# Performance work log

Measured on AMD Instinct MI355X. Metric: run time of the kernel, lower is better.

The kernel has to match this reference:

```python
import jax, jax.numpy as jnp
import numpy as np

N_HEAD = 16


def _rope_cache(T, head_dim):
    half = head_dim // 2
    inv_freq = 1.0 / (10000.0 ** (jnp.arange(half, dtype=jnp.float32) / half))
    t = jnp.arange(T, dtype=jnp.float32)
    freqs = jnp.einsum('i,j->ij', t, inv_freq)            # (T, half)
    cos = jnp.repeat(jnp.cos(freqs), 2, axis=-1)          # (T, head_dim)
    sin = jnp.repeat(jnp.sin(freqs), 2, axis=-1)
    return cos, sin


def _apply_rope(x, cos, sin):
    # x: (B, H, T, D); cos/sin: (T, D)
    x1 = x[..., ::2]
    x2 = x[..., 1::2]
    x_rot = jnp.stack([-x2, x1], axis=-1).reshape(x.shape)
    return x * cos[None, None] + x_rot * sin[None, None]


def setup_inputs() -> dict:
    key = jax.random.key(0)
    k1, k2, k3 = jax.random.split(key, 3)
    B, T, C = 2, 2048, 1024
    x = jax.random.normal(k1, (B, T, C), dtype=jnp.float32)
    Wqkv = jax.random.normal(k2, (C, 3 * C), dtype=jnp.float32) * 0.02
    Wo = jax.random.normal(k3, (C, C), dtype=jnp.float32) * 0.02
    bo = jnp.zeros((C,), dtype=jnp.float32)
    return {"x": x, "Wqkv": Wqkv, "Wo": Wo, "bo": bo}


def reference(x, Wqkv, Wo, bo):
    B, T, C = x.shape
    H = N_HEAD
    D = C // H
    scale = D ** -0.5

    qkv = x @ Wqkv                                        # (B, T, 3C)
    qkv = qkv.reshape(B, T, 3, H, D).transpose(2, 0, 3, 1, 4)  # (3, B, H, T, D)
    q, k, v = qkv[0], qkv[1], qkv[2]

    cos, sin = _rope_cache(T, D)
    q = _apply_rope(q, cos, sin)
    k = _apply_rope(k, cos, sin)

    att = jnp.einsum('bhqd,bhkd->bhqk', q, k) * scale     # (B, H, T, T)
    causal = jnp.tril(jnp.ones((T, T), dtype=bool))
    att = jnp.where(causal[None, None], att, -jnp.inf)
    att = jax.nn.softmax(att, axis=-1)                    # dropout is identity in eval

    out = jnp.einsum('bhqk,bhkd->bhqd', att, v)           # (B, H, T, D)
    out = out.transpose(0, 2, 1, 3).reshape(B, T, C)
    return out @ Wo + bo
```

## Files before the change

### kernel.cpp

```cpp
#include <hip/hip_runtime.h>

typedef __attribute__((ext_vector_type(8))) short bf16x8;
typedef __attribute__((ext_vector_type(4))) float f32x4;
typedef __attribute__((ext_vector_type(4))) unsigned uint32x4;

#define MFMA32(a, b, c) __builtin_amdgcn_mfma_f32_16x16x32_bf16((a), (b), (c), 0, 0, 0)

__device__ __forceinline__ unsigned short f2bf(float f) {
  unsigned u = __builtin_bit_cast(unsigned, f);
  u += 0x7fffu + ((u >> 16) & 1u);
  return (unsigned short)(u >> 16);
}
__device__ __forceinline__ unsigned pack2(float a, float b) {
  return (unsigned)f2bf(a) | ((unsigned)f2bf(b) << 16);
}
__device__ __forceinline__ unsigned pack2t(float lo, float hi) {
  return __builtin_amdgcn_perm(__builtin_bit_cast(unsigned, hi),
                               __builtin_bit_cast(unsigned, lo), 0x07060302u);
}
__device__ __forceinline__ void gl_lds16(const unsigned short* g, unsigned short* l) {
  __builtin_amdgcn_global_load_lds(
      (const __attribute__((address_space(1))) unsigned int*)(g),
      (__attribute__((address_space(3))) unsigned int*)(l), 16, 0, 0);
}

#define QSCALE 0.18033688011112042f

__global__ __launch_bounds__(256) void prep_kernel(
    const float* __restrict__ x, const float* __restrict__ Wqkv,
    const float* __restrict__ Wo, unsigned short* __restrict__ xb,
    unsigned short* __restrict__ wqt, unsigned short* __restrict__ wot) {
  __shared__ unsigned short Tl[64][72];
  const int bid = blockIdx.x, tid = threadIdx.x;
  if (bid < 2048) {
    int i = (bid * 256 + tid) * 8;
    float4 a = *(const float4*)(x + i);
    float4 b = *(const float4*)(x + i + 4);
    uint4 w;
    w.x = pack2(a.x, a.y); w.y = pack2(a.z, a.w);
    w.z = pack2(b.x, b.y); w.w = pack2(b.z, b.w);
    *(uint4*)(xb + i) = w;
  } else {
    const float* src;
    unsigned short* dst;
    int N, kt, nt;
    if (bid < 2816) {
      int r = bid - 2048;
      src = Wqkv; dst = wqt; N = 3072;
      nt = (r % 48) * 64; kt = (r / 48) * 64;
    } else {
      int r = bid - 2816;
      src = Wo; dst = wot; N = 1024;
      nt = (r & 15) * 64; kt = (r >> 4) * 64;
    }
    const int rr = tid >> 2, cs = (tid & 3) * 16;
    const float* sp = src + (kt + rr) * N + nt + cs;
    uint4 w0, w1;
    {
      float4 a = *(const float4*)(sp), b = *(const float4*)(sp + 4);
      float4 c = *(const float4*)(sp + 8), d = *(const float4*)(sp + 12);
      w0.x = pack2(a.x, a.y); w0.y = pack2(a.z, a.w);
      w0.z = pack2(b.x, b.y); w0.w = pack2(b.z, b.w);
      w1.x = pack2(c.x, c.y); w1.y = pack2(c.z, c.w);
      w1.z = pack2(d.x, d.y); w1.w = pack2(d.z, d.w);
    }
    *(uint4*)(&Tl[rr][cs]) = w0;
    *(uint4*)(&Tl[rr][cs + 8]) = w1;
    __syncthreads();
    unsigned short tmp[16];
#pragma unroll
    for (int i = 0; i < 16; i++) tmp[i] = Tl[cs + i][rr];
    unsigned short* dp = dst + (nt + rr) * 1024 + kt + cs;
    *(uint4*)(dp) = *(const uint4*)(&tmp[0]);
    *(uint4*)(dp + 8) = *(const uint4*)(&tmp[8]);
  }
}

__global__ __launch_bounds__(256, 6) void qkv_rope_kernel(
    const unsigned short* __restrict__ xb, const unsigned short* __restrict__ wt,
    unsigned short* __restrict__ qws, unsigned short* __restrict__ kws,
    unsigned short* __restrict__ vws) {
  __shared__ unsigned short Al[2 * 64 * 32];
  __shared__ unsigned short Bl[2 * 128 * 32];

  const int tid = threadIdx.x;
  const int lane = tid & 63, wid = tid >> 6;
  const int quad = lane >> 4, col = lane & 15;
  const int wm = (wid >> 1) * 32, wn = (wid & 1) * 64;
  const int n0 = blockIdx.x * 128, m0 = blockIdx.y * 64;

  f32x4 acc[2][4] = {};
  const int srA = wid * 16 + (lane >> 2);
  const int srB = wid * 32 + (lane >> 2);
  const int gseg = ((lane & 3) ^ ((lane >> 3) & 3)) * 8;
  const int fsg = (quad ^ ((col >> 1) & 3)) * 8;

  for (int k0 = 0; k0 < 1024; k0 += 64) {
#pragma unroll
    for (int c = 0; c < 2; c++) {
      const int kc = k0 + c * 32;
      gl_lds16(xb + (m0 + srA) * 1024 + kc + gseg, Al + c * 2048 + (wid * 16) * 32);
      gl_lds16(wt + (n0 + srB) * 1024 + kc + gseg, Bl + c * 4096 + (wid * 32) * 32);
      gl_lds16(wt + (n0 + srB + 16) * 1024 + kc + gseg,
               Bl + c * 4096 + (wid * 32 + 16) * 32);
    }
    __syncthreads();

#pragma unroll
    for (int c = 0; c < 2; c++) {
      bf16x8 af[2], bfr[4];
#pragma unroll
      for (int i = 0; i < 2; i++)
        af[i] = *(const bf16x8*)(&Al[c * 2048 + (wm + i * 16 + col) * 32 + fsg]);
#pragma unroll
      for (int j = 0; j < 4; j++)
        bfr[j] = *(const bf16x8*)(&Bl[c * 4096 + (wn + j * 16 + col) * 32 + fsg]);
#pragma unroll
      for (int i = 0; i < 2; i++)
#pragma unroll
        for (int j = 0; j < 4; j++)
          acc[i][j] = MFMA32(af[i], bfr[j], acc[i][j]);
    }
    __syncthreads();
  }

#pragma unroll
  for (int i = 0; i < 2; i++) {
#pragma unroll
    for (int j = 0; j < 4; j++) {
      const int nbase = n0 + wn + j * 16;
      const int region = nbase >> 10;
#pragma unroll
      for (int r = 0; r < 4; r++) {
        int m = m0 + wm + i * 16 + quad * 4 + r;
        int n = nbase + col;
        float val = acc[i][j][r];
        int nn = n & 1023, h = nn >> 6, d = nn & 63, b = m >> 11, t = m & 2047;
        if (region < 2) {
          float other = __shfl_xor(val, 1);
          float invf = __expf(-(float)(d >> 1) * 0.28782313662425572f);
          float ang = (float)t * invf;
          float sn, cs;
          __sincosf(ang, &sn, &cs);
          float rot = (d & 1) ? other : -other;
          val = fmaf(val, cs, rot * sn);
        }
        int bh = (b << 4) + h;
        if (region == 0) {
          qws[(bh * 2048 + t) * 64 + d] = f2bf(val * QSCALE);
        } else if (region == 1) {
          kws[(bh * 2048 + t) * 64 + d] = f2bf(val);
        } else {
          int tl = t & 31, g = t >> 5;
          int qd = (tl & 15) >> 2;
          int jj = (tl & 3) + ((tl & 16) ? 4 : 0);
          int tp = g * 32 + qd * 8 + jj;
          vws[(bh * 64 + d) * 2048 + tp] = f2bf(val);
        }
      }
    }
  }
}

__global__ __launch_bounds__(256, 4) void attn_kernel(
    const unsigned short* __restrict__ qws, const unsigned short* __restrict__ kws,
    const unsigned short* __restrict__ vws, unsigned short* __restrict__ aws) {
  __shared__ unsigned short Kl[2][64 * 64];
  __shared__ unsigned short Vl[2][64 * 64];

  const int tid = threadIdx.x;
  const int lane = tid & 63, wid = tid >> 6;
  const int quad = lane >> 4, col = lane & 15;
  const int bh = blockIdx.x;
  const unsigned short* qb = qws + bh * (2048 * 64);
  const unsigned short* kb = kws + bh * (2048 * 64);
  const unsigned short* vb = vws + bh * (64 * 2048);
  const int b = bh >> 4, h = bh & 15;

  const int sro = wid * 16 + (lane >> 3);
  const int sgs = ((lane & 7) ^ ((lane >> 3) & 7)) * 8;
  const int sA = (quad ^ (col & 7)) * 8;

  const int q0blk = (31 - (int)blockIdx.y) * 64;
  const int qt = q0blk + wid * 16;
  const int qi = qt + col;
  const int qi_max = qt + 15;
  const int kend = q0blk + 64;

  bf16x8 qf0 = *(const bf16x8*)(qb + (qt + col) * 64 + quad * 8);
  bf16x8 qf1 = *(const bf16x8*)(qb + (qt + col) * 64 + 32 + quad * 8);

  f32x4 o[4] = {};
  float lsum = 0.f;

  for (int k0 = 0; k0 < kend; k0 += 128) {
    const int nsub = (kend - k0 > 64) ? 2 : 1;
    for (int u = 0; u < nsub; u++) {
      const int kb0 = k0 + u * 64;
      gl_lds16(kb + (kb0 + sro) * 64 + sgs, Kl[u] + (wid * 16) * 64);
      gl_lds16(kb + (kb0 + sro + 8) * 64 + sgs, Kl[u] + (wid * 16 + 8) * 64);
      gl_lds16(vb + sro * 2048 + kb0 + sgs, Vl[u] + (wid * 16) * 64);
      gl_lds16(vb + (sro + 8) * 2048 + kb0 + sgs, Vl[u] + (wid * 16 + 8) * 64);
    }
    __syncthreads();

    for (int u = 0; u < nsub; u++) {
      const int kb0 = k0 + u * 64;
      if (kb0 > qi_max) break;
      const int smax = min(4, ((qi_max - kb0) >> 4) + 1);
      const bool diag = (kb0 + 64 > qt);
      float p[16];
#pragma unroll
      for (int s = 0; s < 4; s++) {
        if (s < smax) {
          bf16x8 kfa = *(const bf16x8*)(&Kl[u][(s * 16 + col) * 64 + sA]);
          bf16x8 kfb = *(const bf16x8*)(&Kl[u][(s * 16 + col) * 64 + (sA ^ 32)]);
          f32x4 z = {0.f, 0.f, 0.f, 0.f};
          z = MFMA32(kfa, qf0, z);
          z = MFMA32(kfb, qf1, z);
          if (diag) {
#pragma unroll
            for (int r = 0; r < 4; r++)
              if (kb0 + s * 16 + quad * 4 + r > qi) z[r] = -1e30f;
          }
#pragma unroll
          for (int r = 0; r < 4; r++) {
            float e = exp2f(z[r]);
            p[s * 4 + r] = e;
            lsum += e;
          }
        } else {
#pragma unroll
          for (int r = 0; r < 4; r++) p[s * 4 + r] = 0.f;
        }
      }
      uint32x4 u0;
      u0[0] = pack2t(p[0], p[1]);   u0[1] = pack2t(p[2], p[3]);
      u0[2] = pack2t(p[4], p[5]);   u0[3] = pack2t(p[6], p[7]);
      bf16x8 pf0 = __builtin_bit_cast(bf16x8, u0);
#pragma unroll
      for (int dt = 0; dt < 4; dt++) {
        bf16x8 vfa = *(const bf16x8*)(&Vl[u][(dt * 16 + col) * 64 + sA]);
        o[dt] = MFMA32(vfa, pf0, o[dt]);
      }
      if (smax > 2) {
        uint32x4 u1;
        u1[0] = pack2t(p[8], p[9]);   u1[1] = pack2t(p[10], p[11]);
        u1[2] = pack2t(p[12], p[13]); u1[3] = pack2t(p[14], p[15]);
        bf16x8 pf1 = __builtin_bit_cast(bf16x8, u1);
#pragma unroll
        for (int dt = 0; dt < 4; dt++) {
          bf16x8 vfb = *(const bf16x8*)(&Vl[u][(dt * 16 + col) * 64 + (sA ^ 32)]);
          o[dt] = MFMA32(vfb, pf1, o[dt]);
        }
      }
    }
    __syncthreads();
  }

  lsum += __shfl_xor(lsum, 16);
  lsum += __shfl_xor(lsum, 32);
  float inv = 1.0f / lsum;
#pragma unroll
  for (int dt = 0; dt < 4; dt++)
#pragma unroll
    for (int r = 0; r < 4; r++) {
      int d = dt * 16 + quad * 4 + r;
      aws[(b * 2048 + qt + col) * 1024 + h * 64 + d] = f2bf(o[dt][r] * inv);
    }
}

__global__ __launch_bounds__(256) void out_proj_kernel(
    const unsigned short* __restrict__ attn, const unsigned short* __restrict__ wot,
    const float* __restrict__ bo, float* __restrict__ out) {
  __shared__ unsigned short Al[2 * 64 * 32];
  __shared__ unsigned short Bl[2 * 128 * 32];

  const int tid = threadIdx.x;
  const int lane = tid & 63, wid = tid >> 6;
  const int quad = lane >> 4, col = lane & 15;
  const int wm = (wid >> 1) * 32, wn = (wid & 1) * 64;
  const int n0 = blockIdx.x * 128, m0 = blockIdx.y * 64;

  f32x4 acc[2][4] = {};
  const int sr = lane >> 2;
  const int gseg = ((lane & 3) ^ ((lane >> 3) & 3)) * 8;
  const int fsg = (quad ^ ((col >> 1) & 3)) * 8;

  for (int k0 = 0; k0 < 1024; k0 += 64) {
#pragma unroll
    for (int c = 0; c < 2; c++) {
      const int kc = k0 + c * 32;
      gl_lds16(attn + (m0 + wid * 16 + sr) * 1024 + kc + gseg,
               Al + c * 2048 + (wid * 16) * 32);
      gl_lds16(wot + (n0 + wid * 32 + sr) * 1024 + kc + gseg,
               Bl + c * 4096 + (wid * 32) * 32);
      gl_lds16(wot + (n0 + wid * 32 + 16 + sr) * 1024 + kc + gseg,
               Bl + c * 4096 + (wid * 32 + 16) * 32);
    }
    __syncthreads();

#pragma unroll
    for (int c = 0; c < 2; c++) {
      bf16x8 af[2], bfr[4];
#pragma unroll
      for (int i = 0; i < 2; i++)
        af[i] = *(const bf16x8*)(&Al[c * 2048 + (wm + i * 16 + col) * 32 + fsg]);
#pragma unroll
      for (int j = 0; j < 4; j++)
        bfr[j] = *(const bf16x8*)(&Bl[c * 4096 + (wn + j * 16 + col) * 32 + fsg]);
#pragma unroll
      for (int i = 0; i < 2; i++)
#pragma unroll
        for (int j = 0; j < 4; j++)
          acc[i][j] = MFMA32(af[i], bfr[j], acc[i][j]);
    }
    __syncthreads();
  }

#pragma unroll
  for (int i = 0; i < 2; i++)
#pragma unroll
    for (int j = 0; j < 4; j++)
#pragma unroll
      for (int r = 0; r < 4; r++) {
        int m = m0 + wm + i * 16 + quad * 4 + r;
        int n = n0 + wn + j * 16 + col;
        out[m * 1024 + n] = acc[i][j][r] + bo[n];
      }
}

extern "C" void kernel_launch(void* const* d_in, const int* in_sizes, int n_in,
                              void* d_out, int out_size, void* d_ws, size_t ws_size,
                              hipStream_t stream) {
  const float* x = (const float*)d_in[0];
  const float* Wqkv = (const float*)d_in[1];
  const float* Wo = (const float*)d_in[2];
  const float* bo = (const float*)d_in[3];
  float* out = (float*)d_out;

  unsigned short* qws = (unsigned short*)d_ws;
  unsigned short* kws = qws + 4194304;
  unsigned short* vws = kws + 4194304;
  unsigned short* xb  = vws + 4194304;
  unsigned short* aws = xb;
  unsigned short* wqt = xb + 4194304;
  unsigned short* wot = wqt + 3145728;

  prep_kernel<<<3072, 256, 0, stream>>>(x, Wqkv, Wo, xb, wqt, wot);
  qkv_rope_kernel<<<dim3(24, 64), 256, 0, stream>>>(xb, wqt, qws, kws, vws);
  attn_kernel<<<dim3(32, 32), 256, 0, stream>>>(qws, kws, vws, aws);
  out_proj_kernel<<<dim3(8, 64), 256, 0, stream>>>(aws, wot, bo, out);
}
```

Baseline: 183.8 us.

## Process two 16-row query tiles per wave to reuse K/V LDS fragments

Each wave now handles 32 query rows as two 16-row tiles instead of one. K and V fragments read from LDS are shared between both tiles, and the grid's y dimension is halved so each block covers a 128-row query slab. MFMA sections are wrapped in s_setprio raises to favour matrix issue. This cuts LDS reads and K/V global loads per query row, at the cost of more registers (launch bounds lowered to 2), fewer blocks, and more wasted masked work on the diagonal.

```diff
diff --git a/kernel.cpp b/kernel.cpp
--- a/kernel.cpp
+++ b/kernel.cpp
@@ -162,7 +162,7 @@
   }
 }
 
-__global__ __launch_bounds__(256, 4) void attn_kernel(
+__global__ __launch_bounds__(256, 2) void attn_kernel(
     const unsigned short* __restrict__ qws, const unsigned short* __restrict__ kws,
     const unsigned short* __restrict__ vws, unsigned short* __restrict__ aws) {
   __shared__ unsigned short Kl[2][64 * 64];
@@ -181,21 +181,24 @@
   const int sgs = ((lane & 7) ^ ((lane >> 3) & 7)) * 8;
   const int sA = (quad ^ (col & 7)) * 8;
 
-  const int q0blk = (31 - (int)blockIdx.y) * 64;
-  const int qt = q0blk + wid * 16;
-  const int qi = qt + col;
-  const int qi_max = qt + 15;
-  const int kend = q0blk + 64;
-
-  bf16x8 qf0 = *(const bf16x8*)(qb + (qt + col) * 64 + quad * 8);
-  bf16x8 qf1 = *(const bf16x8*)(qb + (qt + col) * 64 + 32 + quad * 8);
-
-  f32x4 o[4] = {};
-  float lsum = 0.f;
+  const int slab = (15 - (int)blockIdx.y) * 128;
+  const int qt0 = slab + wid * 32;
+  const int qt1 = qt0 + 16;
+  const int qi0 = qt0 + col, qi1 = qt1 + col;
+  const int qimax0 = qt0 + 15, qimax1 = qt1 + 15;
+  const int kend = slab + 128;
+
+  bf16x8 qf0a = *(const bf16x8*)(qb + (qt0 + col) * 64 + quad * 8);
+  bf16x8 qf0b = *(const bf16x8*)(qb + (qt0 + col) * 64 + 32 + quad * 8);
+  bf16x8 qf1a = *(const bf16x8*)(qb + (qt1 + col) * 64 + quad * 8);
+  bf16x8 qf1b = *(const bf16x8*)(qb + (qt1 + col) * 64 + 32 + quad * 8);
+
+  f32x4 o0[4] = {}, o1[4] = {};
+  float ls0 = 0.f, ls1 = 0.f;
 
   for (int k0 = 0; k0 < kend; k0 += 128) {
-    const int nsub = (kend - k0 > 64) ? 2 : 1;
-    for (int u = 0; u < nsub; u++) {
+#pragma unroll
+    for (int u = 0; u < 2; u++) {
       const int kb0 = k0 + u * 64;
       gl_lds16(kb + (kb0 + sro) * 64 + sgs, Kl[u] + (wid * 16) * 64);
       gl_lds16(kb + (kb0 + sro + 8) * 64 + sgs, Kl[u] + (wid * 16 + 8) * 64);
@@ -204,69 +207,163 @@
     }
     __syncthreads();
 
-    for (int u = 0; u < nsub; u++) {
+    for (int u = 0; u < 2; u++) {
       const int kb0 = k0 + u * 64;
-      if (kb0 > qi_max) break;
-      const int smax = min(4, ((qi_max - kb0) >> 4) + 1);
-      const bool diag = (kb0 + 64 > qt);
-      float p[16];
-#pragma unroll
-      for (int s = 0; s < 4; s++) {
-        if (s < smax) {
+      if (kb0 > qimax1) break;
+      int d0 = (qimax0 - kb0) >> 4;
+      const int smax0 = min(4, max(0, d0 + 1));
+      const int smax1 = min(4, ((qimax1 - kb0) >> 4) + 1);
+      const bool diag0 = (kb0 + 64 > qt0);
+      const bool diag1 = (kb0 + 64 > qt1);
+      float p0[8], p1[8];
+
+#pragma unroll
+      for (int s = 0; s < 2; s++) {
+        bf16x8 kfa = *(const bf16x8*)(&Kl[u][(s * 16 + col) * 64 + sA]);
+        bf16x8 kfb = *(const bf16x8*)(&Kl[u][(s * 16 + col) * 64 + (sA ^ 32)]);
+        if (s < smax0) {
+          f32x4 z = {0.f, 0.f, 0.f, 0.f};
+          __builtin_amdgcn_s_setprio(1);
+          z = MFMA32(kfa, qf0a, z);
+          z = MFMA32(kfb, qf0b, z);
+          __builtin_amdgcn_s_setprio(0);
+          if (diag0) {
+#pragma unroll
+            for (int r = 0; r < 4; r++)
+              if (kb0 + s * 16 + quad * 4 + r > qi0) z[r] = -1e30f;
+          }
+#pragma unroll
+          for (int r = 0; r < 4; r++) {
+            float e = exp2f(z[r]);
+            p0[s * 4 + r] = e;
+            ls0 += e;
+          }
+        } else {
+#pragma unroll
+          for (int r = 0; r < 4; r++) p0[s * 4 + r] = 0.f;
+        }
+        if (s < smax1) {
+          f32x4 z = {0.f, 0.f, 0.f, 0.f};
+          __builtin_amdgcn_s_setprio(1);
+          z = MFMA32(kfa, qf1a, z);
+          z = MFMA32(kfb, qf1b, z);
+          __builtin_amdgcn_s_setprio(0);
+          if (diag1) {
+#pragma unroll
+            for (int r = 0; r < 4; r++)
+              if (kb0 + s * 16 + quad * 4 + r > qi1) z[r] = -1e30f;
+          }
+#pragma unroll
+          for (int r = 0; r < 4; r++) {
+            float e = exp2f(z[r]);
+            p1[s * 4 + r] = e;
+            ls1 += e;
+          }
+        } else {
+#pragma unroll
+          for (int r = 0; r < 4; r++) p1[s * 4 + r] = 0.f;
+        }
+      }
+      {
+        uint32x4 w0, w1;
+        w0[0] = pack2t(p0[0], p0[1]); w0[1] = pack2t(p0[2], p0[3]);
+        w0[2] = pack2t(p0[4], p0[5]); w0[3] = pack2t(p0[6], p0[7]);
+        w1[0] = pack2t(p1[0], p1[1]); w1[1] = pack2t(p1[2], p1[3]);
+        w1[2] = pack2t(p1[4], p1[5]); w1[3] = pack2t(p1[6], p1[7]);
+        bf16x8 pg0 = __builtin_bit_cast(bf16x8, w0);
+        bf16x8 pg1 = __builtin_bit_cast(bf16x8, w1);
+        __builtin_amdgcn_s_setprio(1);
+#pragma unroll
+        for (int dt = 0; dt < 4; dt++) {
+          bf16x8 vfa = *(const bf16x8*)(&Vl[u][(dt * 16 + col) * 64 + sA]);
+          o0[dt] = MFMA32(vfa, pg0, o0[dt]);
+          o1[dt] = MFMA32(vfa, pg1, o1[dt]);
+        }
+        __builtin_amdgcn_s_setprio(0);
+      }
+
+      if (smax1 > 2) {
+#pragma unroll
+        for (int s = 2; s < 4; s++) {
           bf16x8 kfa = *(const bf16x8*)(&Kl[u][(s * 16 + col) * 64 + sA]);
           bf16x8 kfb = *(const bf16x8*)(&Kl[u][(s * 16 + col) * 64 + (sA ^ 32)]);
-          f32x4 z = {0.f, 0.f, 0.f, 0.f};
-          z = MFMA32(kfa, qf0, z);
-          z = MFMA32(kfb, qf1, z);
-          if (diag) {
-#pragma unroll
-            for (int r = 0; r < 4; r++)
-              if (kb0 + s * 16 + quad * 4 + r > qi) z[r] = -1e30f;
-          }
-#pragma unroll
-          for (int r = 0; r < 4; r++) {
-            float e = exp2f(z[r]);
-            p[s * 4 + r] = e;
-            lsum += e;
-          }
-        } else {
-#pragma unroll
-          for (int r = 0; r < 4; r++) p[s * 4 + r] = 0.f;
-        }
-      }
-      uint32x4 u0;
-      u0[0] = pack2t(p[0], p[1]);   u0[1] = pack2t(p[2], p[3]);
-      u0[2] = pack2t(p[4], p[5]);   u0[3] = pack2t(p[6], p[7]);
-      bf16x8 pf0 = __builtin_bit_cast(bf16x8, u0);
-#pragma unroll
-      for (int dt = 0; dt < 4; dt++) {
-        bf16x8 vfa = *(const bf16x8*)(&Vl[u][(dt * 16 + col) * 64 + sA]);
-        o[dt] = MFMA32(vfa, pf0, o[dt]);
-      }
-      if (smax > 2) {
-        uint32x4 u1;
-        u1[0] = pack2t(p[8], p[9]);   u1[1] = pack2t(p[10], p[11]);
-        u1[2] = pack2t(p[12], p[13]); u1[3] = pack2t(p[14], p[15]);
-        bf16x8 pf1 = __builtin_bit_cast(bf16x8, u1);
+          if (s < smax0) {
+            f32x4 z = {0.f, 0.f, 0.f, 0.f};
+            __builtin_amdgcn_s_setprio(1);
+            z = MFMA32(kfa, qf0a, z);
+            z = MFMA32(kfb, qf0b, z);
+            __builtin_amdgcn_s_setprio(0);
+            if (diag0) {
+#pragma unroll
+              for (int r = 0; r < 4; r++)
+                if (kb0 + s * 16 + quad * 4 + r > qi0) z[r] = -1e30f;
+            }
+#pragma unroll
+            for (int r = 0; r < 4; r++) {
+              float e = exp2f(z[r]);
+              p0[(s - 2) * 4 + r] = e;
+              ls0 += e;
+            }
+          } else {
+#pragma unroll
+            for (int r = 0; r < 4; r++) p0[(s - 2) * 4 + r] = 0.f;
+          }
+          if (s < smax1) {
+            f32x4 z = {0.f, 0.f, 0.f, 0.f};
+            __builtin_amdgcn_s_setprio(1);
+            z = MFMA32(kfa, qf1a, z);
+            z = MFMA32(kfb, qf1b, z);
+            __builtin_amdgcn_s_setprio(0);
+            if (diag1) {
+#pragma unroll
+              for (int r = 0; r < 4; r++)
+                if (kb0 + s * 16 + quad * 4 + r > qi1) z[r] = -1e30f;
+            }
+#pragma unroll
+            for (int r = 0; r < 4; r++) {
+              float e = exp2f(z[r]);
+              p1[(s - 2) * 4 + r] = e;
+              ls1 += e;
+            }
+          } else {
+#pragma unroll
+            for (int r = 0; r < 4; r++) p1[(s - 2) * 4 + r] = 0.f;
+          }
+        }
+        uint32x4 w0, w1;
+        w0[0] = pack2t(p0[0], p0[1]); w0[1] = pack2t(p0[2], p0[3]);
+        w0[2] = pack2t(p0[4], p0[5]); w0[3] = pack2t(p0[6], p0[7]);
+        w1[0] = pack2t(p1[0], p1[1]); w1[1] = pack2t(p1[2], p1[3]);
+        w1[2] = pack2t(p1[4], p1[5]); w1[3] = pack2t(p1[6], p1[7]);
+        bf16x8 pg0 = __builtin_bit_cast(bf16x8, w0);
+        bf16x8 pg1 = __builtin_bit_cast(bf16x8, w1);
+        const bool g0b = (smax0 > 2);
+        __builtin_amdgcn_s_setprio(1);
 #pragma unroll
         for (int dt = 0; dt < 4; dt++) {
           bf16x8 vfb = *(const bf16x8*)(&Vl[u][(dt * 16 + col) * 64 + (sA ^ 32)]);
-          o[dt] = MFMA32(vfb, pf1, o[dt]);
-        }
+          if (g0b) o0[dt] = MFMA32(vfb, pg0, o0[dt]);
+          o1[dt] = MFMA32(vfb, pg1, o1[dt]);
+        }
+        __builtin_amdgcn_s_setprio(0);
       }
     }
     __syncthreads();
   }
 
-  lsum += __shfl_xor(lsum, 16);
-  lsum += __shfl_xor(lsum, 32);
-  float inv = 1.0f / lsum;
+  ls0 += __shfl_xor(ls0, 16);
+  ls0 += __shfl_xor(ls0, 32);
+  ls1 += __shfl_xor(ls1, 16);
+  ls1 += __shfl_xor(ls1, 32);
+  float inv0 = 1.0f / ls0;
+  float inv1 = 1.0f / ls1;
 #pragma unroll
   for (int dt = 0; dt < 4; dt++)
 #pragma unroll
     for (int r = 0; r < 4; r++) {
       int d = dt * 16 + quad * 4 + r;
-      aws[(b * 2048 + qt + col) * 1024 + h * 64 + d] = f2bf(o[dt][r] * inv);
+      aws[(b * 2048 + qt0 + col) * 1024 + h * 64 + d] = f2bf(o0[dt][r] * inv0);
+      aws[(b * 2048 + qt1 + col) * 1024 + h * 64 + d] = f2bf(o1[dt][r] * inv1);
     }
 }
 
@@ -349,6 +446,6 @@
 
   prep_kernel<<<3072, 256, 0, stream>>>(x, Wqkv, Wo, xb, wqt, wot);
   qkv_rope_kernel<<<dim3(24, 64), 256, 0, stream>>>(xb, wqt, qws, kws, vws);
-  attn_kernel<<<dim3(32, 32), 256, 0, stream>>>(qws, kws, vws, aws);
+  attn_kernel<<<dim3(32, 16), 256, 0, stream>>>(qws, kws, vws, aws);
   out_proj_kernel<<<dim3(8, 64), 256, 0, stream>>>(aws, wot, bo, out);
 }
```

New measurement: 201.8 us. +9.8%, slower.
